# Performance work log

Measured on AMD Instinct MI355X. Metric: run time of the kernel, lower is better.

Reference implementation:

```python
import jax, jax.numpy as jnp
import numpy as np

B, S, D = 4, 2048, 768
H = 12
HD = D // H  # 64
SCALE = HD ** -0.5

def setup_inputs() -> dict:
    key = jax.random.key(0)
    k1, k2, k3 = jax.random.split(key, 3)
    x = jax.random.normal(k1, (B, S, D), dtype=jnp.float32)
    w_qkv = jax.random.normal(k2, (D, 3 * D), dtype=jnp.float32) * (D ** -0.5)
    w_out = jax.random.normal(k3, (D, D), dtype=jnp.float32) * (D ** -0.5)
    b_out = jnp.zeros((D,), dtype=jnp.float32)
    return {"x": x, "w_qkv": w_qkv, "w_out": w_out, "b_out": b_out}

def reference(x, w_qkv, w_out, b_out):
    B_, S_, D_ = x.shape
    # qkv projection (no bias), then 'b s (qkv h d) -> qkv b h s d'
    qkv = (x @ w_qkv).reshape(B_, S_, 3, H, HD).transpose(2, 0, 3, 1, 4)
    q, k, v = qkv[0], qkv[1], qkv[2]  # each [B, H, S, HD]
    att = jnp.einsum('bhxd,bhyd->bhxy', q, k) * SCALE
    att = jax.nn.softmax(att, axis=-1)  # dropout_rate=0 -> identity
    out = jnp.einsum('bhxy,bhyd->bhxd', att, v)
    out = out.transpose(0, 2, 1, 3).reshape(B_, S_, D_)  # 'b h s d -> b s (h d)'
    return out @ w_out + b_out
```

## Files before the change

kernel.cpp:

```cpp
#include <hip/hip_runtime.h>

#define BB 4
#define SS 2048
#define DD 768
#define HH 12
#define HDIM 64

using bf16_t = __bf16;
typedef __bf16 bf16x8 __attribute__((ext_vector_type(8)));
typedef __bf16 bf16x4 __attribute__((ext_vector_type(4)));
typedef __bf16 bf16x2 __attribute__((ext_vector_type(2)));
typedef float f32x4 __attribute__((ext_vector_type(4)));
typedef float f32x16 __attribute__((ext_vector_type(16)));
typedef unsigned int u32;
typedef unsigned int u32x4 __attribute__((ext_vector_type(4)));

static __device__ __forceinline__ void cp16(void* lds, const void* g) {
  __builtin_amdgcn_global_load_lds(
      (const __attribute__((address_space(1))) u32*)g,
      (__attribute__((address_space(3))) u32*)lds, 16, 0, 0);
}

__global__ void cvt_x(const float* __restrict__ in, bf16_t* __restrict__ out) {
  const size_t i = ((size_t)blockIdx.x * 256 + threadIdx.x) * 8;
  f32x4 f0 = *(const f32x4*)(in + i);
  f32x4 f1 = *(const f32x4*)(in + i + 4);
  bf16x8 v;
#pragma unroll
  for (int j = 0; j < 4; j++) { v[j] = (bf16_t)f0[j]; v[4 + j] = (bf16_t)f1[j]; }
  *(bf16x8*)(out + i) = v;
}

__global__ void wt_transpose(const float* __restrict__ in, bf16_t* __restrict__ out,
                             int K, int N) {
  __shared__ bf16_t tile[64][65];
  const int n0 = blockIdx.x * 64, k0 = blockIdx.y * 64;
  const int t = threadIdx.x;
  const int r = t >> 2;
  const int c0 = (t & 3) * 16;
  const float* src = in + (size_t)(k0 + r) * N + n0 + c0;
#pragma unroll
  for (int q = 0; q < 4; q++) {
    f32x4 f = *(const f32x4*)(src + q * 4);
#pragma unroll
    for (int j = 0; j < 4; j++) tile[r][c0 + q * 4 + j] = (bf16_t)f[j];
  }
  __syncthreads();
  bf16x8 o0, o1;
#pragma unroll
  for (int j = 0; j < 8; j++) { o0[j] = tile[c0 + j][r]; o1[j] = tile[c0 + 8 + j][r]; }
  *(bf16x8*)(out + (size_t)(n0 + r) * K + k0 + c0) = o0;
  *(bf16x8*)(out + (size_t)(n0 + r) * K + k0 + c0 + 8) = o1;
}

__global__ __launch_bounds__(512, 2)
void gemm_qkv(const bf16_t* __restrict__ A, const bf16_t* __restrict__ Bt,
              bf16_t* __restrict__ q_out, bf16_t* __restrict__ k_out,
              bf16_t* __restrict__ vt_out) {
  __shared__ bf16_t As[2][256][32];
  __shared__ bf16_t Bs[2][256][32];
  const int t = threadIdx.x;
  const int lane = t & 63, wave = t >> 6;
  const int l15 = lane & 15, quad = lane >> 4;
  const int wm = (wave >> 2) * 128, wn = (wave & 3) * 64;
  const int K = DD;

  const int L = blockIdx.y * 9 + blockIdx.x;
  const int v = (L & 7) * 36 + (L >> 3);
  const int m0 = (v / 9) * 256, n0 = (v % 9) * 256;

  const int drow = lane >> 2;
  const int dcol = ((lane & 3) ^ ((lane >> 3) & 3)) * 8;
  const int rxor = (l15 >> 1) & 3;

  f32x4 acc[8][4];
#pragma unroll
  for (int i = 0; i < 8; i++)
#pragma unroll
    for (int j = 0; j < 4; j++) acc[i][j] = (f32x4){0.f, 0.f, 0.f, 0.f};

  auto stage = [&](int k0, int buf) {
#pragma unroll
    for (int c = 0; c < 2; c++) {
      const int row = wave * 32 + c * 16 + drow;
      cp16(&As[buf][wave * 32 + c * 16][0],
           A + (size_t)(m0 + row) * K + k0 + dcol);
      cp16(&Bs[buf][wave * 32 + c * 16][0],
           Bt + (size_t)(n0 + row) * K + k0 + dcol);
    }
  };

  const int NT = K / 32;
  stage(0, 0);

  for (int kt = 0; kt < NT; kt++) {
    const int buf = kt & 1;
    __syncthreads();
    if (kt + 1 < NT) stage((kt + 1) * 32, buf ^ 1);
    bf16x8 af[8], bfr[4];
#pragma unroll
    for (int i = 0; i < 8; i++)
      af[i] = *(const bf16x8*)&As[buf][wm + i * 16 + l15][(quad ^ rxor) * 8];
#pragma unroll
    for (int j = 0; j < 4; j++)
      bfr[j] = *(const bf16x8*)&Bs[buf][wn + j * 16 + l15][(quad ^ rxor) * 8];
#pragma unroll
    for (int i = 0; i < 8; i++)
#pragma unroll
      for (int j = 0; j < 4; j++)
        acc[i][j] = __builtin_amdgcn_mfma_f32_16x16x32_bf16(af[i], bfr[j], acc[i][j], 0, 0, 0);
  }

  const float QSCALE = 0.125f * 1.44269504088896340736f;
#pragma unroll
  for (int i = 0; i < 8; i++) {
    const int mbase = m0 + wm + i * 16 + quad * 4;
#pragma unroll
    for (int j = 0; j < 4; j++) {
      const int n = n0 + wn + j * 16 + l15;
#pragma unroll
      for (int r = 0; r < 4; r++) {
        const float v = acc[i][j][r];
        const int mm = mbase + r;
        const int sel = n / DD;
        const int rem = n - sel * DD;
        const int h = rem >> 6, d = rem & 63;
        const int b = mm >> 11, s = mm & 2047;
        if (sel == 2) {
          vt_out[((size_t)(b * HH + h) * HDIM + d) * SS + s] = (bf16_t)v;
        } else {
          const size_t idx = (((size_t)(b * HH + h)) * SS + s) * HDIM + d;
          if (sel == 0) q_out[idx] = (bf16_t)(v * QSCALE);
          else k_out[idx] = (bf16_t)v;
        }
      }
    }
  }
}

__global__ __launch_bounds__(256, 2)
void gemm_proj(const bf16_t* __restrict__ A, const bf16_t* __restrict__ Bt,
               float* __restrict__ Cout, const float* __restrict__ bias) {
  __shared__ bf16_t As[2][128][64];
  __shared__ bf16_t Bs[2][128][64];
  const int t = threadIdx.x;
  const int lane = t & 63, wave = t >> 6;
  const int l15 = lane & 15, quad = lane >> 4;
  const int wm = (wave >> 1) * 64, wn = (wave & 1) * 64;
  const int K = DD, N = DD;

  const int nx = gridDim.x;
  const int L = blockIdx.y * nx + blockIdx.x;
  const int chunk = (nx * gridDim.y) >> 3;
  const int v = (L & 7) * chunk + (L >> 3);
  const int m0 = (v / nx) * 128, n0 = (v % nx) * 128;

  const int srow = lane >> 3;
  const int schunk = ((lane & 7) ^ srow) * 8;
  const int rsw = l15 & 7;

  f32x4 acc[4][4];
#pragma unroll
  for (int i = 0; i < 4; i++)
#pragma unroll
    for (int j = 0; j < 4; j++) acc[i][j] = (f32x4){0.f, 0.f, 0.f, 0.f};

  auto stage = [&](int k0, int buf) {
#pragma unroll
    for (int p = 0; p < 4; p++) {
      const int row = wave * 32 + p * 8 + srow;
      const int mm = m0 + row, b = mm >> 11, s = mm & 2047, h = k0 >> 6;
      cp16(&As[buf][wave * 32 + p * 8][0],
           A + (((size_t)(b * HH + h)) * SS + s) * HDIM + schunk);
      cp16(&Bs[buf][wave * 32 + p * 8][0],
           Bt + (size_t)(n0 + row) * K + k0 + schunk);
    }
  };

  const int NT = K / 64;
  stage(0, 0);

  for (int kt = 0; kt < NT; kt++) {
    const int buf = kt & 1;
    __syncthreads();
    if (kt + 1 < NT) stage((kt + 1) * 64, buf ^ 1);
#pragma unroll
    for (int kk = 0; kk < 2; kk++) {
      bf16x8 af[4], bfr[4];
#pragma unroll
      for (int i = 0; i < 4; i++)
        af[i] = *(const bf16x8*)&As[buf][wm + i * 16 + l15][((kk * 4 + quad) ^ rsw) * 8];
#pragma unroll
      for (int j = 0; j < 4; j++)
        bfr[j] = *(const bf16x8*)&Bs[buf][wn + j * 16 + l15][((kk * 4 + quad) ^ rsw) * 8];
#pragma unroll
      for (int i = 0; i < 4; i++)
#pragma unroll
        for (int j = 0; j < 4; j++)
          acc[i][j] = __builtin_amdgcn_mfma_f32_16x16x32_bf16(af[i], bfr[j], acc[i][j], 0, 0, 0);
    }
  }

#pragma unroll
  for (int i = 0; i < 4; i++) {
    const int mbase = m0 + wm + i * 16 + quad * 4;
#pragma unroll
    for (int j = 0; j < 4; j++) {
      const int n = n0 + wn + j * 16 + l15;
#pragma unroll
      for (int r = 0; r < 4; r++)
        Cout[(size_t)(mbase + r) * N + n] = acc[i][j][r] + bias[n];
    }
  }
}

__global__ __launch_bounds__(256, 3)
void attn_kernel(bf16_t* __restrict__ Qio, const bf16_t* __restrict__ Kg,
                 const bf16_t* __restrict__ Vt) {
  __shared__ bf16_t Ks[2][64][64];
  __shared__ bf16_t Vts[2][64][64];
  __shared__ float lsum[128];
  const int t = threadIdx.x;
  const int lane = t & 63, wave = t >> 6;
  const int l31 = lane & 31, hi = lane >> 5;

  const int L = blockIdx.y * gridDim.x + blockIdx.x;
  const int v = (L & 7) * ((16 * BB * HH) / 8) + (L >> 3);
  const int bh = v >> 4;
  const int q0 = (v & 15) * 128;

  const size_t base = (size_t)bh * SS * HDIM;
  const size_t baset = (size_t)bh * HDIM * SS;
  const int wq = wave * 32;
  const int srow = lane >> 3;
  const int rsw = (l31 & 7) ^ (l31 >> 3);

  bf16x8 qf[4];
#pragma unroll
  for (int kd = 0; kd < 4; kd++)
    qf[kd] = *(const bf16x8*)(Qio + base + (size_t)(q0 + wq + l31) * HDIM +
                              kd * 16 + hi * 8);

  float l_lane = 0.f;
  f32x16 o_acc[2];
#pragma unroll
  for (int dt = 0; dt < 2; dt++)
#pragma unroll
    for (int r = 0; r < 16; r++) o_acc[dt][r] = 0.f;

  f32x16 sA[2], sB[2];

  auto stageK = [&](int k0, int buf) {
#pragma unroll
    for (int p = 0; p < 2; p++) {
      const int sc = ((lane & 7) ^ srow ^ ((wave * 2 + p) & 3)) * 8;
      cp16(&Ks[buf][wave * 16 + p * 8][0],
           Kg + base + (size_t)(k0 + wave * 16 + p * 8 + srow) * HDIM + sc);
    }
  };
  auto stageV = [&](int k0, int buf) {
#pragma unroll
    for (int p = 0; p < 2; p++) {
      const int sc = ((lane & 7) ^ srow ^ ((wave * 2 + p) & 3)) * 8;
      cp16(&Vts[buf][wave * 16 + p * 8][0],
           Vt + baset + (size_t)(wave * 16 + p * 8 + srow) * SS + k0 + sc);
    }
  };

  auto qk = [&](int buf, f32x16 (&s)[2]) {
    __builtin_amdgcn_s_setprio(1);
#pragma unroll
    for (int ct = 0; ct < 2; ct++) {
#pragma unroll
      for (int r = 0; r < 16; r++) s[ct][r] = 0.f;
#pragma unroll
      for (int kd = 0; kd < 4; kd++) {
        bf16x8 kf = *(const bf16x8*)&Ks[buf][ct * 32 + l31][((2 * kd + hi) ^ rsw) * 8];
        s[ct] = __builtin_amdgcn_mfma_f32_32x32x16_bf16(kf, qf[kd], s[ct], 0, 0, 0);
      }
    }
    __builtin_amdgcn_s_setprio(0);
  };

  auto smpv = [&](int buf, const f32x16 (&sT)[2]) {
    bf16x8 pa[4];
#pragma unroll
    for (int ct = 0; ct < 2; ct++) {
      float p[16];
#pragma unroll
      for (int r = 0; r < 16; r++) p[r] = __builtin_amdgcn_exp2f(sT[ct][r]);
#pragma unroll
      for (int r = 0; r < 16; r += 4)
        l_lane += (p[r] + p[r + 1]) + (p[r + 2] + p[r + 3]);
      u32 w[4][2];
#pragma unroll
      for (int g = 0; g < 4; g++)
#pragma unroll
        for (int i = 0; i < 2; i++) {
          bf16x2 pk = {(bf16_t)p[4 * g + 2 * i], (bf16_t)p[4 * g + 2 * i + 1]};
          w[g][i] = *(u32*)&pk;
        }
#pragma unroll
      for (int sub = 0; sub < 2; sub++) {
        u32 a0 = w[2 * sub][0], b0 = w[2 * sub + 1][0];
        u32 a1 = w[2 * sub][1], b1 = w[2 * sub + 1][1];
        asm volatile("v_permlane32_swap_b32 %0, %1" : "+v"(a0), "+v"(b0));
        asm volatile("v_permlane32_swap_b32 %0, %1" : "+v"(a1), "+v"(b1));
        u32x4 fr = {a0, a1, b0, b1};
        pa[ct * 2 + sub] = *(bf16x8*)&fr;
      }
    }
    __builtin_amdgcn_s_setprio(1);
#pragma unroll
    for (int kk = 0; kk < 4; kk++)
#pragma unroll
      for (int dt = 0; dt < 2; dt++) {
        bf16x8 vf = *(const bf16x8*)&Vts[buf][dt * 32 + l31][((2 * kk + hi) ^ rsw) * 8];
        o_acc[dt] = __builtin_amdgcn_mfma_f32_32x32x16_bf16(pa[kk], vf, o_acc[dt], 0, 0, 0);
      }
    __builtin_amdgcn_s_setprio(0);
  };

  stageK(0, 0); stageK(64, 1); stageV(0, 0);
  __syncthreads();
  qk(0, sA);
  __syncthreads();

#pragma unroll 1
  for (int it = 0; it < 30; it += 2) {
    stageK((it + 2) * 64, 0);
    stageV((it + 1) * 64, 1);
    qk(1, sB);
    smpv(0, sA);
    __syncthreads();
    stageK((it + 3) * 64, 1);
    stageV((it + 2) * 64, 0);
    qk(0, sA);
    smpv(1, sB);
    __syncthreads();
  }
  stageV(31 * 64, 1);
  qk(1, sB);
  smpv(0, sA);
  __syncthreads();
  smpv(1, sB);

  const float lf = l_lane + __shfl_xor(l_lane, 32);
  lsum[wq + l31] = lf;
#pragma unroll
  for (int r = 0; r < 16; r++) {
    const int q = wq + (r & 3) + 8 * (r >> 2) + 4 * hi;
    const float inv = 1.0f / lsum[q];
#pragma unroll
    for (int dt = 0; dt < 2; dt++) {
      const int d = dt * 32 + l31;
      Qio[base + (size_t)(q0 + q) * HDIM + d] = (bf16_t)(o_acc[dt][r] * inv);
    }
  }
}

extern "C" void kernel_launch(void* const* d_in, const int* in_sizes, int n_in,
                              void* d_out, int out_size, void* d_ws, size_t ws_size,
                              hipStream_t stream) {
  const float* x = (const float*)d_in[0];
  const float* w_qkv = (const float*)d_in[1];
  const float* w_out = (const float*)d_in[2];
  const float* b_out = (const float*)d_in[3];
  float* out = (float*)d_out;

  char* ws = (char*)d_ws;
  bf16_t* wqkv_t = (bf16_t*)ws; ws += (size_t)3 * DD * DD * 2;
  bf16_t* wout_t = (bf16_t*)ws; ws += (size_t)DD * DD * 2;
  bf16_t* q_ws = (bf16_t*)ws;   ws += (size_t)BB * HH * SS * HDIM * 2;
  bf16_t* k_ws = (bf16_t*)ws;
  bf16_t* vt_sc = (bf16_t*)d_out;
  bf16_t* xb = (bf16_t*)d_out + (size_t)BB * SS * DD;

  cvt_x<<<(BB * SS * DD) / (256 * 8), 256, 0, stream>>>(x, xb);
  wt_transpose<<<dim3(3 * DD / 64, DD / 64), 256, 0, stream>>>(w_qkv, wqkv_t, DD, 3 * DD);
  wt_transpose<<<dim3(DD / 64, DD / 64), 256, 0, stream>>>(w_out, wout_t, DD, DD);
  gemm_qkv<<<dim3((3 * DD) / 256, (BB * SS) / 256), 512, 0, stream>>>(
      xb, wqkv_t, q_ws, k_ws, vt_sc);
  attn_kernel<<<dim3(SS / 128, BB * HH), 256, 0, stream>>>(q_ws, k_ws, vt_sc);
  gemm_proj<<<dim3(DD / 128, (BB * SS) / 128), 256, 0, stream>>>(
      q_ws, wout_t, out, b_out);
}
```

Before: 262.8 us.

## Deepen QKV GEMM K-tile to 64 with split-phase staged loads and priority MFMA

The QKV projection GEMM now uses a K-tile of 64 instead of 32, which halves the number of main-loop iterations and barriers. It uses a new 8-chunk XOR swizzle for the LDS layout. Each iteration is split into four compute phases, and the next tile's B and A loads are interleaved between them, with explicit vmcnt waits and raw s_barrier in place of __syncthreads. MFMA blocks are wrapped in s_setprio to favour compute issue. This doubles LDS use per block (128 KB), which may limit occupancy, and relies on hand-tuned waitcnt counts being correct.

```diff
diff --git a/kernel.cpp b/kernel.cpp
--- a/kernel.cpp
+++ b/kernel.cpp
@@ -57,8 +57,8 @@
 void gemm_qkv(const bf16_t* __restrict__ A, const bf16_t* __restrict__ Bt,
               bf16_t* __restrict__ q_out, bf16_t* __restrict__ k_out,
               bf16_t* __restrict__ vt_out) {
-  __shared__ bf16_t As[2][256][32];
-  __shared__ bf16_t Bs[2][256][32];
+  __shared__ bf16_t As[2][256][64];
+  __shared__ bf16_t Bs[2][256][64];
   const int t = threadIdx.x;
   const int lane = t & 63, wave = t >> 6;
   const int l15 = lane & 15, quad = lane >> 4;
@@ -69,9 +69,9 @@
   const int v = (L & 7) * 36 + (L >> 3);
   const int m0 = (v / 9) * 256, n0 = (v % 9) * 256;
 
-  const int drow = lane >> 2;
-  const int dcol = ((lane & 3) ^ ((lane >> 3) & 3)) * 8;
-  const int rxor = (l15 >> 1) & 3;
+  const int srow = lane >> 3;
+  const int schunk = ((lane & 7) ^ srow) * 8;
+  const int rsw = l15 & 7;
 
   f32x4 acc[8][4];
 #pragma unroll
@@ -79,36 +79,71 @@
 #pragma unroll
     for (int j = 0; j < 4; j++) acc[i][j] = (f32x4){0.f, 0.f, 0.f, 0.f};
 
-  auto stage = [&](int k0, int buf) {
-#pragma unroll
-    for (int c = 0; c < 2; c++) {
-      const int row = wave * 32 + c * 16 + drow;
-      cp16(&As[buf][wave * 32 + c * 16][0],
-           A + (size_t)(m0 + row) * K + k0 + dcol);
-      cp16(&Bs[buf][wave * 32 + c * 16][0],
-           Bt + (size_t)(n0 + row) * K + k0 + dcol);
-    }
-  };
-
-  const int NT = K / 32;
-  stage(0, 0);
+  auto stageA = [&](int kt, int ca, int cb) {
+    const int buf = kt & 1, k0 = kt * 64;
+#pragma unroll
+    for (int cc = 0; cc < 2; cc++) {
+      const int c = cc ? cb : ca;
+      cp16(&As[buf][(c * 8 + wave) * 8][0],
+           A + (size_t)(m0 + (c * 8 + wave) * 8 + srow) * K + k0 + schunk);
+    }
+  };
+  auto stageB = [&](int kt, int ca, int cb) {
+    const int buf = kt & 1, k0 = kt * 64;
+#pragma unroll
+    for (int cc = 0; cc < 2; cc++) {
+      const int c = cc ? cb : ca;
+      cp16(&Bs[buf][(c * 8 + wave) * 8][0],
+           Bt + (size_t)(n0 + (c * 8 + wave) * 8 + srow) * K + k0 + schunk);
+    }
+  };
+
+  auto phase = [&](int buf, int q) {
+    bf16x8 af[2][2], bfr[4][2];
+#pragma unroll
+    for (int il = 0; il < 2; il++)
+#pragma unroll
+      for (int kk = 0; kk < 2; kk++)
+        af[il][kk] = *(const bf16x8*)&As[buf][wm + (q * 2 + il) * 16 + l15]
+                                            [((kk * 4 + quad) ^ rsw) * 8];
+#pragma unroll
+    for (int j = 0; j < 4; j++)
+#pragma unroll
+      for (int kk = 0; kk < 2; kk++)
+        bfr[j][kk] = *(const bf16x8*)&Bs[buf][wn + j * 16 + l15]
+                                            [((kk * 4 + quad) ^ rsw) * 8];
+    __builtin_amdgcn_s_setprio(1);
+#pragma unroll
+    for (int il = 0; il < 2; il++)
+#pragma unroll
+      for (int j = 0; j < 4; j++)
+#pragma unroll
+        for (int kk = 0; kk < 2; kk++)
+          acc[q * 2 + il][j] = __builtin_amdgcn_mfma_f32_16x16x32_bf16(
+              af[il][kk], bfr[j][kk], acc[q * 2 + il][j], 0, 0, 0);
+    __builtin_amdgcn_s_setprio(0);
+  };
+
+  const int NT = K / 64;
+  stageB(0, 0, 1); stageB(0, 2, 3); stageA(0, 0, 2); stageA(0, 1, 3);
 
   for (int kt = 0; kt < NT; kt++) {
     const int buf = kt & 1;
-    __syncthreads();
-    if (kt + 1 < NT) stage((kt + 1) * 32, buf ^ 1);
-    bf16x8 af[8], bfr[4];
-#pragma unroll
-    for (int i = 0; i < 8; i++)
-      af[i] = *(const bf16x8*)&As[buf][wm + i * 16 + l15][(quad ^ rxor) * 8];
-#pragma unroll
-    for (int j = 0; j < 4; j++)
-      bfr[j] = *(const bf16x8*)&Bs[buf][wn + j * 16 + l15][(quad ^ rxor) * 8];
-#pragma unroll
-    for (int i = 0; i < 8; i++)
-#pragma unroll
-      for (int j = 0; j < 4; j++)
-        acc[i][j] = __builtin_amdgcn_mfma_f32_16x16x32_bf16(af[i], bfr[j], acc[i][j], 0, 0, 0);
+    asm volatile("s_waitcnt vmcnt(2)" ::: "memory");
+    __builtin_amdgcn_s_barrier();
+    __builtin_amdgcn_sched_barrier(0);
+    if (kt + 1 < NT) stageB(kt + 1, 0, 1);
+    phase(buf, 0);
+    if (kt + 1 < NT) stageB(kt + 1, 2, 3);
+    phase(buf, 1);
+    if (kt + 1 < NT) { asm volatile("s_waitcnt vmcnt(4)" ::: "memory"); }
+    else             { asm volatile("s_waitcnt vmcnt(0)" ::: "memory"); }
+    __builtin_amdgcn_s_barrier();
+    __builtin_amdgcn_sched_barrier(0);
+    if (kt + 1 < NT) stageA(kt + 1, 0, 2);
+    phase(buf, 2);
+    if (kt + 1 < NT) stageA(kt + 1, 1, 3);
+    phase(buf, 3);
   }
 
   const float QSCALE = 0.125f * 1.44269504088896340736f;
@@ -120,18 +155,18 @@
       const int n = n0 + wn + j * 16 + l15;
 #pragma unroll
       for (int r = 0; r < 4; r++) {
-        const float v = acc[i][j][r];
+        const float vv = acc[i][j][r];
         const int mm = mbase + r;
         const int sel = n / DD;
         const int rem = n - sel * DD;
         const int h = rem >> 6, d = rem & 63;
         const int b = mm >> 11, s = mm & 2047;
         if (sel == 2) {
-          vt_out[((size_t)(b * HH + h) * HDIM + d) * SS + s] = (bf16_t)v;
+          vt_out[((size_t)(b * HH + h) * HDIM + d) * SS + s] = (bf16_t)vv;
         } else {
           const size_t idx = (((size_t)(b * HH + h)) * SS + s) * HDIM + d;
-          if (sel == 0) q_out[idx] = (bf16_t)(v * QSCALE);
-          else k_out[idx] = (bf16_t)v;
+          if (sel == 0) q_out[idx] = (bf16_t)(vv * QSCALE);
+          else k_out[idx] = (bf16_t)vv;
         }
       }
     }
```

Result: no change. 263.6 us (+0.3%).
